# Kernel optimization log

Measured on AMD Instinct MI355X. Metric: run time of the kernel, lower is better.

## Reference

```python
import jax, jax.numpy as jnp
import numpy as np

D_IN = 128
D_HID = 256


def _mlp(x, W1, b1, W2, b2):
    # two-layer MLP with ReLU (dropout is identity at eval)
    h = jax.nn.relu(x @ W1 + b1)
    return jax.nn.relu(h @ W2 + b2)


def setup_inputs() -> dict:
    key = jax.random.key(0)
    kA, kB, k1, k2, k3, k4 = jax.random.split(key, 6)
    A = jax.random.normal(kA, (4, 4096, D_IN), dtype=jnp.float32)
    B = jax.random.normal(kB, (4, 4096, D_IN), dtype=jnp.float32)
    s1 = 1.0 / np.sqrt(D_IN)
    s2 = 1.0 / np.sqrt(D_HID)
    W1 = jax.random.uniform(k1, (D_IN, D_HID), jnp.float32, -s1, s1)
    b1 = jax.random.uniform(k2, (D_HID,), jnp.float32, -s1, s1)
    W2 = jax.random.uniform(k3, (D_HID, D_HID), jnp.float32, -s2, s2)
    b2 = jax.random.uniform(k4, (D_HID,), jnp.float32, -s2, s2)
    return {"A": A, "B": B, "W1": W1, "b1": b1, "W2": W2, "b2": b2}


def reference(A, B, W1, b1, W2, b2):
    f_A = _mlp(A, W1, b1, W2, b2)  # [b, m, h]
    f_B = _mlp(B, W1, b1, W2, b2)  # [b, n, h]
    e = jnp.einsum('bmh,bnh->bmn', f_A, f_B)  # unscaled scores
    beta = jnp.einsum('bmn,bnd->bmd', jax.nn.softmax(e, axis=-1), B)
    alpha = jnp.einsum('bmn,bmd->bnd', jax.nn.softmax(e, axis=-2), A)
    return (beta, alpha)
```

## Files before the change

### kernel.cpp

```cpp
#include <hip/hip_runtime.h>

typedef __attribute__((ext_vector_type(8))) short bf16x8;
typedef __attribute__((ext_vector_type(4))) float f32x4;
typedef __attribute__((ext_vector_type(16))) float f32x16;

__device__ __forceinline__ ushort f2bf(float x) {
  union { float f; unsigned u; } c; c.f = x;
  unsigned u = c.u;
  u += 0x7fffu + ((u >> 16) & 1u);
  return (ushort)(u >> 16);
}

__device__ __forceinline__ unsigned cvt_pk_bf16(float lo, float hi) {
  unsigned r;
  asm("v_cvt_pk_bf16_f32 %0, %1, %2" : "=v"(r) : "v"(lo), "v"(hi));
  return r;
}

__device__ __forceinline__ void gl_lds16(const void* g, void* s) {
  __builtin_amdgcn_global_load_lds(
      (const __attribute__((address_space(1))) unsigned*)g,
      (__attribute__((address_space(3))) unsigned*)s, 16, 0, 0);
}

__global__ __launch_bounds__(256) void prep_w(
    const float* __restrict__ W1, const float* __restrict__ W2,
    ushort* __restrict__ Wt1, ushort* __restrict__ Wt2)
{
  int idx = blockIdx.x * 256 + threadIdx.x;
  if (idx < 32768) {
    int k = idx >> 8, n = idx & 255;
    Wt1[n * 128 + k] = f2bf(W1[idx]);
  }
  {
    int k = idx >> 8, n = idx & 255;
    Wt2[n * 256 + k] = f2bf(W2[idx]);
  }
}

__global__ __launch_bounds__(256) void fused_mlp(
    const float* __restrict__ A, const float* __restrict__ Bm,
    const ushort* __restrict__ Wt1, const float* __restrict__ b1,
    const ushort* __restrict__ Wt2, const float* __restrict__ b2,
    ushort* __restrict__ fA, ushort* __restrict__ fB,
    ushort* __restrict__ At, ushort* __restrict__ Bt)
{
  const float* X = blockIdx.y ? Bm : A;
  ushort* outF = blockIdx.y ? fB : fA;
  ushort* outT = blockIdx.y ? Bt : At;

  __shared__ ushort Xl[64][136];
  __shared__ ushort Hl[64][264];

  int tid = threadIdx.x;
  int l = tid & 63, w = tid >> 6;
  int rowbase = blockIdx.x * 64 + w * 16;

  bf16x8 xf[4];
  {
    int r = rowbase + (l & 15);
    int koff = (l >> 4) * 8;
    const float* Xp = X + (size_t)r * 128 + koff;
#pragma unroll
    for (int kc = 0; kc < 4; ++kc) {
      float4 a = *(const float4*)(Xp + kc * 32);
      float4 c = *(const float4*)(Xp + kc * 32 + 4);
      bf16x8 v;
      v[0] = (short)f2bf(a.x); v[1] = (short)f2bf(a.y);
      v[2] = (short)f2bf(a.z); v[3] = (short)f2bf(a.w);
      v[4] = (short)f2bf(c.x); v[5] = (short)f2bf(c.y);
      v[6] = (short)f2bf(c.z); v[7] = (short)f2bf(c.w);
      xf[kc] = v;
      *(bf16x8*)&Xl[w * 16 + (l & 15)][koff + kc * 32] = v;
    }
  }

  f32x4 acc1[16];
#pragma unroll
  for (int i = 0; i < 16; ++i) acc1[i] = (f32x4){0.f, 0.f, 0.f, 0.f};
#pragma unroll
  for (int kc = 0; kc < 4; ++kc) {
#pragma unroll
    for (int nf = 0; nf < 16; ++nf) {
      bf16x8 bfv = *(const bf16x8*)&Wt1[(size_t)(nf * 16 + (l & 15)) * 128 + kc * 32 + (l >> 4) * 8];
      acc1[nf] = __builtin_amdgcn_mfma_f32_16x16x32_bf16(xf[kc], bfv, acc1[nf], 0, 0, 0);
    }
  }
  __syncthreads();

  {
    int b = (blockIdx.x * 64) >> 12;
    int m0 = (blockIdx.x * 64) & 4095;
    int d = tid >> 1, mh = (tid & 1) * 32;
    ushort* op = outT + ((size_t)b * 128 + d) * 4096 + m0 + mh;
#pragma unroll
    for (int g = 0; g < 4; ++g) {
      bf16x8 v;
#pragma unroll
      for (int j = 0; j < 8; ++j) v[j] = (short)Xl[mh + g * 8 + j][d];
      *(bf16x8*)(op + g * 8) = v;
    }
  }

#pragma unroll
  for (int nf = 0; nf < 16; ++nf) {
    int col = nf * 16 + (l & 15);
    float bv = b1[col];
#pragma unroll
    for (int i = 0; i < 4; ++i) {
      float v = fmaxf(acc1[nf][i] + bv, 0.f);
      Hl[w * 16 + (l >> 4) * 4 + i][col] = f2bf(v);
    }
  }
  __syncthreads();

  bf16x8 hf[8];
  {
    int koff = (l >> 4) * 8;
#pragma unroll
    for (int kc = 0; kc < 8; ++kc)
      hf[kc] = *(const bf16x8*)&Hl[w * 16 + (l & 15)][koff + kc * 32];
  }
  f32x4 acc2[16];
#pragma unroll
  for (int i = 0; i < 16; ++i) acc2[i] = (f32x4){0.f, 0.f, 0.f, 0.f};
#pragma unroll
  for (int kc = 0; kc < 8; ++kc) {
#pragma unroll
    for (int nf = 0; nf < 16; ++nf) {
      bf16x8 bfv = *(const bf16x8*)&Wt2[(size_t)(nf * 16 + (l & 15)) * 256 + kc * 32 + (l >> 4) * 8];
      acc2[nf] = __builtin_amdgcn_mfma_f32_16x16x32_bf16(hf[kc], bfv, acc2[nf], 0, 0, 0);
    }
  }
#pragma unroll
  for (int nf = 0; nf < 16; ++nf) {
    int col = nf * 16 + (l & 15);
    float bv = b2[col];
#pragma unroll
    for (int i = 0; i < 4; ++i) {
      float v = fmaxf(acc2[nf][i] + bv, 0.f);
      outF[(size_t)(rowbase + (l >> 4) * 4 + i) * 256 + col] = f2bf(v);
    }
  }
}

__global__ __launch_bounds__(256, 2) void flash2(
    const ushort* __restrict__ fA, const ushort* __restrict__ fB,
    const ushort* __restrict__ At, const ushort* __restrict__ Bt,
    float* __restrict__ out)
{
  int bp = blockIdx.x;
  int pass = bp >> 2, b = bp & 3;
  int qbase = blockIdx.y * 64;
  const ushort* fQ = pass ? fB : fA;
  const ushort* fK = pass ? fA : fB;
  const ushort* Vg = pass ? At : Bt;
  float* O = out + (size_t)pass * (4u * 4096 * 128) + (size_t)b * 4096 * 128;

  __shared__ ushort Kl[2][64 * 256];

  int tid = threadIdx.x;
  int l = tid & 63, w = tid >> 6;
  int l31 = l & 31, g5 = l >> 5;
  int qw = w & 1, kw = w >> 1;

  const size_t fkbase = (size_t)b * 4096 * 256;
  const size_t vgbase = (size_t)b * 128 * 4096;

  auto stage_k = [&](int t_, int buf_) {
    const ushort* kp = fK + fkbase + (size_t)t_ * 16384;
    ushort* lb = &Kl[buf_][0] + w * 4096;
#pragma unroll
    for (int s = 0; s < 8; ++s) {
      int row = w * 16 + s * 2 + g5;
      int gs = l31 ^ (row & 7);
      gl_lds16(kp + (size_t)row * 256 + gs * 8, lb + s * 512);
    }
  };

  bf16x8 q[16];
  {
    const ushort* qp = fQ + fkbase + (size_t)(qbase + qw * 32 + l31) * 256 + g5 * 8;
#pragma unroll
    for (int kc = 0; kc < 16; ++kc) q[kc] = *(const bf16x8*)(qp + kc * 16);
  }

  f32x16 acc_o0 = {}, acc_o1 = {}, acc_o2 = {}, acc_o3 = {};
  float m_run = -INFINITY, l_run = 0.f;

  stage_k(0, 0);

  for (int t = 0; t < 64; ++t) {
    int cur = t & 1;
    __syncthreads();
    if (t < 63) stage_k(t + 1, cur ^ 1);

    bf16x8 vv[2][4];
#pragma unroll
    for (int dblk = 0; dblk < 4; ++dblk) {
      const ushort* vp = Vg + vgbase + (size_t)(dblk * 32 + l31) * 4096
                         + t * 64 + kw * 32 + g5 * 8;
#pragma unroll
      for (int kblk = 0; kblk < 2; ++kblk)
        vv[kblk][dblk] = *(const bf16x8*)(vp + kblk * 16);
    }

    const ushort* kbuf = &Kl[cur][0];
    int krow = kw * 32 + l31;
    int sx = l31 & 7;
    f32x16 s0 = {}, s1 = {};
#pragma unroll
    for (int kc = 0; kc < 8; ++kc) {
      bf16x8 a0 = *(const bf16x8*)&kbuf[krow * 256 + (((4 * kc + g5) ^ sx) * 8)];
      bf16x8 a1 = *(const bf16x8*)&kbuf[krow * 256 + (((4 * kc + 2 + g5) ^ sx) * 8)];
      s0 = __builtin_amdgcn_mfma_f32_32x32x16_bf16(a0, q[2 * kc],     s0, 0, 0, 0);
      s1 = __builtin_amdgcn_mfma_f32_32x32x16_bf16(a1, q[2 * kc + 1], s1, 0, 0, 0);
    }

    float sv[16];
#pragma unroll
    for (int r = 0; r < 16; ++r) sv[r] = s0[r] + s1[r];

    float pmax = sv[0];
#pragma unroll
    for (int r = 1; r < 16; ++r) pmax = fmaxf(pmax, sv[r]);
    pmax = fmaxf(pmax, __shfl_xor(pmax, 32));

    if (!__all(pmax <= m_run + 8.f)) {
      float mnew = fmaxf(m_run, pmax);
      float sc = __expf(m_run - mnew);
      l_run *= sc;
#pragma unroll
      for (int r = 0; r < 16; ++r) {
        float scr = __shfl(sc, (r & 3) + 8 * (r >> 2) + 4 * g5);
        acc_o0[r] *= scr; acc_o1[r] *= scr; acc_o2[r] *= scr; acc_o3[r] *= scr;
      }
      m_run = mnew;
    }

    float p[16], psum = 0.f;
#pragma unroll
    for (int r = 0; r < 16; ++r) {
      p[r] = __expf(sv[r] - m_run);
      psum += p[r];
    }
    l_run += psum + __shfl_xor(psum, 32);

    unsigned pk[4][2];
#pragma unroll
    for (int r2 = 0; r2 < 4; ++r2) {
      pk[r2][0] = cvt_pk_bf16(p[4 * r2 + 0], p[4 * r2 + 1]);
      pk[r2][1] = cvt_pk_bf16(p[4 * r2 + 2], p[4 * r2 + 3]);
    }

#pragma unroll
    for (int kblk = 0; kblk < 2; ++kblk) {
      int r2a = 2 * kblk, r2b = r2a + 1;
      unsigned la0 = pk[r2a][0], la1 = pk[r2a][1];
      unsigned lb0 = pk[r2b][0], lb1 = pk[r2b][1];
      unsigned s0w = g5 ? la0 : lb0, s1w = g5 ? la1 : lb1;
      unsigned rc0 = (unsigned)__shfl_xor((int)s0w, 32);
      unsigned rc1 = (unsigned)__shfl_xor((int)s1w, 32);
      union { unsigned u[4]; bf16x8 v; } pf;
      pf.u[0] = g5 ? rc0 : la0;  pf.u[1] = g5 ? rc1 : la1;
      pf.u[2] = g5 ? lb0 : rc0;  pf.u[3] = g5 ? lb1 : rc1;
      acc_o0 = __builtin_amdgcn_mfma_f32_32x32x16_bf16(pf.v, vv[kblk][0], acc_o0, 0, 0, 0);
      acc_o1 = __builtin_amdgcn_mfma_f32_32x32x16_bf16(pf.v, vv[kblk][1], acc_o1, 0, 0, 0);
      acc_o2 = __builtin_amdgcn_mfma_f32_32x32x16_bf16(pf.v, vv[kblk][2], acc_o2, 0, 0, 0);
      acc_o3 = __builtin_amdgcn_mfma_f32_32x32x16_bf16(pf.v, vv[kblk][3], acc_o3, 0, 0, 0);
    }
  }

  __syncthreads();
  float* shm = (float*)&Kl[0][0];
  shm[w * 128 + l] = m_run;
  shm[w * 128 + 64 + l] = l_run;
  {
    float* sa = shm + 512 + w * 2048;
    const f32x16& send0 = kw ? acc_o0 : acc_o2;
    const f32x16& send1 = kw ? acc_o1 : acc_o3;
#pragma unroll
    for (int r = 0; r < 16; ++r) {
      sa[r * 64 + l] = send0[r];
      sa[1024 + r * 64 + l] = send1[r];
    }
  }
  __syncthreads();
  {
    int pw = w ^ 2;
    float m1 = shm[pw * 128 + l];
    float l1 = shm[pw * 128 + 64 + l];
    float M = fmaxf(m_run, m1);
    float a0 = __expf(m_run - M), a1 = __expf(m1 - M);
    float inv = 1.f / (l_run * a0 + l1 * a1);
    const float* sp = shm + 512 + pw * 2048;
    const f32x16& keep0 = kw ? acc_o2 : acc_o0;
    const f32x16& keep1 = kw ? acc_o3 : acc_o1;
    int dbase = kw ? 64 : 0;
    int qr = qbase + qw * 32;
#pragma unroll
    for (int r = 0; r < 16; ++r) {
      int rowl = (r & 3) + 8 * (r >> 2) + 4 * g5;
      float invr = __shfl(inv, rowl);
      float a0r = __shfl(a0, rowl);
      float a1r = __shfl(a1, rowl);
      float* op = O + (size_t)(qr + rowl) * 128 + dbase + l31;
      op[0]  = (keep0[r] * a0r + sp[r * 64 + l] * a1r) * invr;
      op[32] = (keep1[r] * a0r + sp[1024 + r * 64 + l] * a1r) * invr;
    }
  }
}

extern "C" void kernel_launch(void* const* d_in, const int* in_sizes, int n_in,
                              void* d_out, int out_size, void* d_ws, size_t ws_size,
                              hipStream_t stream) {
  const float* A  = (const float*)d_in[0];
  const float* Bm = (const float*)d_in[1];
  const float* W1 = (const float*)d_in[2];
  const float* b1 = (const float*)d_in[3];
  const float* W2 = (const float*)d_in[4];
  const float* b2 = (const float*)d_in[5];
  float* out = (float*)d_out;

  ushort* ws = (ushort*)d_ws;
  ushort* fA  = ws;
  ushort* fB  = fA + 4194304;
  ushort* At  = fB + 4194304;
  ushort* Bt  = At + 2097152;
  ushort* Wt1 = Bt + 2097152;
  ushort* Wt2 = Wt1 + 32768;

  prep_w<<<256, 256, 0, stream>>>(W1, W2, Wt1, Wt2);
  fused_mlp<<<dim3(256, 2), 256, 0, stream>>>(A, Bm, Wt1, b1, Wt2, b2,
                                              fA, fB, At, Bt);
  flash2<<<dim3(8, 64), 256, 0, stream>>>(fA, fB, At, Bt, out);
}
```

Before: 233.3 us.

## Split flash attention over key chunks with fp16 partials and merge kernel

Replaces the single flash kernel with a split-K variant. Each block now has 512 threads, 128 query rows and one quarter of the keys. Each block writes normalized fp16 partial outputs plus per-row max and sum to workspace, and a separate merge kernel combines the four partials with log-sum-exp weights. The two passes run as separate launches that reuse the same partial buffers. The aim is more parallelism and fewer serial key iterations per block. The cost is extra global traffic, four launches instead of one, and fp16 rounding of the partial results.

```diff
diff --git a/kernel.cpp b/kernel.cpp
--- a/kernel.cpp
+++ b/kernel.cpp
@@ -144,45 +144,49 @@
   }
 }
 
-__global__ __launch_bounds__(256, 2) void flash2(
+__global__ __launch_bounds__(512, 4) void flashV(
     const ushort* __restrict__ fA, const ushort* __restrict__ fB,
     const ushort* __restrict__ At, const ushort* __restrict__ Bt,
-    float* __restrict__ out)
+    _Float16* __restrict__ Pf16, float* __restrict__ pML, int pass)
 {
-  int bp = blockIdx.x;
-  int pass = bp >> 2, b = bp & 3;
-  int qbase = blockIdx.y * 64;
+  int bx = blockIdx.x;
+  int b = bx >> 2, kc = bx & 3;
+  int qblk = blockIdx.y;
   const ushort* fQ = pass ? fB : fA;
   const ushort* fK = pass ? fA : fB;
   const ushort* Vg = pass ? At : Bt;
-  float* O = out + (size_t)pass * (4u * 4096 * 128) + (size_t)b * 4096 * 128;
-
-  __shared__ ushort Kl[2][64 * 256];
+  _Float16* P = Pf16 + (size_t)kc * 2097152 + (size_t)b * 524288;
+  float* pml = pML + ((size_t)kc * 4 + b) * 8192;
+
+  __shared__ ushort Kl[2][16384];
+  __shared__ float mlsh[1024];
 
   int tid = threadIdx.x;
   int l = tid & 63, w = tid >> 6;
   int l31 = l & 31, g5 = l >> 5;
-  int qw = w & 1, kw = w >> 1;
+  int qg = w >> 1, kw = w & 1;
 
   const size_t fkbase = (size_t)b * 4096 * 256;
   const size_t vgbase = (size_t)b * 128 * 4096;
+  const int key0 = kc * 1024;
 
   auto stage_k = [&](int t_, int buf_) {
-    const ushort* kp = fK + fkbase + (size_t)t_ * 16384;
-    ushort* lb = &Kl[buf_][0] + w * 4096;
-#pragma unroll
-    for (int s = 0; s < 8; ++s) {
-      int row = w * 16 + s * 2 + g5;
-      int gs = l31 ^ (row & 7);
+    const ushort* kp = fK + fkbase + (size_t)(key0 + t_ * 64) * 256;
+    ushort* lb = &Kl[buf_][0] + w * 2048;
+#pragma unroll
+    for (int s = 0; s < 4; ++s) {
+      int row = w * 8 + s * 2 + g5;
+      int gs = l31 ^ (row & 31);
       gl_lds16(kp + (size_t)row * 256 + gs * 8, lb + s * 512);
     }
   };
 
   bf16x8 q[16];
   {
-    const ushort* qp = fQ + fkbase + (size_t)(qbase + qw * 32 + l31) * 256 + g5 * 8;
-#pragma unroll
-    for (int kc = 0; kc < 16; ++kc) q[kc] = *(const bf16x8*)(qp + kc * 16);
+    const ushort* qp = fQ + fkbase
+        + (size_t)(qblk * 128 + qg * 32 + l31) * 256 + g5 * 8;
+#pragma unroll
+    for (int kq = 0; kq < 16; ++kq) q[kq] = *(const bf16x8*)(qp + kq * 16);
   }
 
   f32x16 acc_o0 = {}, acc_o1 = {}, acc_o2 = {}, acc_o3 = {};
@@ -190,31 +194,29 @@
 
   stage_k(0, 0);
 
-  for (int t = 0; t < 64; ++t) {
+  for (int t = 0; t < 16; ++t) {
     int cur = t & 1;
     __syncthreads();
-    if (t < 63) stage_k(t + 1, cur ^ 1);
+    if (t < 15) stage_k(t + 1, cur ^ 1);
 
     bf16x8 vv[2][4];
 #pragma unroll
     for (int dblk = 0; dblk < 4; ++dblk) {
       const ushort* vp = Vg + vgbase + (size_t)(dblk * 32 + l31) * 4096
-                         + t * 64 + kw * 32 + g5 * 8;
-#pragma unroll
-      for (int kblk = 0; kblk < 2; ++kblk)
-        vv[kblk][dblk] = *(const bf16x8*)(vp + kblk * 16);
+                         + key0 + t * 64 + kw * 32 + g5 * 8;
+      vv[0][dblk] = *(const bf16x8*)(vp);
+      vv[1][dblk] = *(const bf16x8*)(vp + 16);
     }
 
     const ushort* kbuf = &Kl[cur][0];
     int krow = kw * 32 + l31;
-    int sx = l31 & 7;
     f32x16 s0 = {}, s1 = {};
 #pragma unroll
-    for (int kc = 0; kc < 8; ++kc) {
-      bf16x8 a0 = *(const bf16x8*)&kbuf[krow * 256 + (((4 * kc + g5) ^ sx) * 8)];
-      bf16x8 a1 = *(const bf16x8*)&kbuf[krow * 256 + (((4 * kc + 2 + g5) ^ sx) * 8)];
-      s0 = __builtin_amdgcn_mfma_f32_32x32x16_bf16(a0, q[2 * kc],     s0, 0, 0, 0);
-      s1 = __builtin_amdgcn_mfma_f32_32x32x16_bf16(a1, q[2 * kc + 1], s1, 0, 0, 0);
+    for (int kq = 0; kq < 8; ++kq) {
+      bf16x8 a0 = *(const bf16x8*)&kbuf[krow * 256 + (((4 * kq + g5)     ^ l31) * 8)];
+      bf16x8 a1 = *(const bf16x8*)&kbuf[krow * 256 + (((4 * kq + 2 + g5) ^ l31) * 8)];
+      s0 = __builtin_amdgcn_mfma_f32_32x32x16_bf16(a0, q[2 * kq],     s0, 0, 0, 0);
+      s1 = __builtin_amdgcn_mfma_f32_32x32x16_bf16(a1, q[2 * kq + 1], s1, 0, 0, 0);
     }
 
     float sv[16];
@@ -272,11 +274,11 @@
   }
 
   __syncthreads();
-  float* shm = (float*)&Kl[0][0];
-  shm[w * 128 + l] = m_run;
-  shm[w * 128 + 64 + l] = l_run;
-  {
-    float* sa = shm + 512 + w * 2048;
+  mlsh[w * 128 + l] = m_run;
+  mlsh[w * 128 + 64 + l] = l_run;
+  float* accsh = (float*)&Kl[0][0];
+  {
+    float* sa = accsh + w * 2048;
     const f32x16& send0 = kw ? acc_o0 : acc_o2;
     const f32x16& send1 = kw ? acc_o1 : acc_o3;
 #pragma unroll
@@ -287,28 +289,65 @@
   }
   __syncthreads();
   {
-    int pw = w ^ 2;
-    float m1 = shm[pw * 128 + l];
-    float l1 = shm[pw * 128 + 64 + l];
+    int pw = w ^ 1;
+    float m1 = mlsh[pw * 128 + l];
+    float l1 = mlsh[pw * 128 + 64 + l];
     float M = fmaxf(m_run, m1);
     float a0 = __expf(m_run - M), a1 = __expf(m1 - M);
-    float inv = 1.f / (l_run * a0 + l1 * a1);
-    const float* sp = shm + 512 + pw * 2048;
+    float lsum = l_run * a0 + l1 * a1;
+    float inv = 1.f / lsum;
+    const float* sp = accsh + pw * 2048;
     const f32x16& keep0 = kw ? acc_o2 : acc_o0;
     const f32x16& keep1 = kw ? acc_o3 : acc_o1;
     int dbase = kw ? 64 : 0;
-    int qr = qbase + qw * 32;
+    int qr = qblk * 128 + qg * 32;
+    if (kw == 0 && g5 == 0) {
+      pml[qr + l31] = M;
+      pml[4096 + qr + l31] = lsum;
+    }
 #pragma unroll
     for (int r = 0; r < 16; ++r) {
       int rowl = (r & 3) + 8 * (r >> 2) + 4 * g5;
       float invr = __shfl(inv, rowl);
       float a0r = __shfl(a0, rowl);
       float a1r = __shfl(a1, rowl);
-      float* op = O + (size_t)(qr + rowl) * 128 + dbase + l31;
-      op[0]  = (keep0[r] * a0r + sp[r * 64 + l] * a1r) * invr;
-      op[32] = (keep1[r] * a0r + sp[1024 + r * 64 + l] * a1r) * invr;
-    }
-  }
+      _Float16* op = P + (size_t)(qr + rowl) * 128 + dbase + l31;
+      op[0]  = (_Float16)((keep0[r] * a0r + sp[r * 64 + l] * a1r) * invr);
+      op[32] = (_Float16)((keep1[r] * a0r + sp[1024 + r * 64 + l] * a1r) * invr);
+    }
+  }
+}
+
+__global__ __launch_bounds__(256) void kmerge4(
+    float* __restrict__ outp, const _Float16* __restrict__ Pf16,
+    const float* __restrict__ pML)
+{
+  size_t i = ((size_t)blockIdx.x * 256 + threadIdx.x) * 4;
+  int fr = (int)(i >> 7);
+  int b = fr >> 12, row = fr & 4095;
+
+  float m0 = pML[((size_t)0 * 4 + b) * 8192 + row];
+  float m1 = pML[((size_t)1 * 4 + b) * 8192 + row];
+  float m2 = pML[((size_t)2 * 4 + b) * 8192 + row];
+  float m3 = pML[((size_t)3 * 4 + b) * 8192 + row];
+  float M = fmaxf(fmaxf(m0, m1), fmaxf(m2, m3));
+  float w0 = __expf(m0 - M) * pML[((size_t)0 * 4 + b) * 8192 + 4096 + row];
+  float w1 = __expf(m1 - M) * pML[((size_t)1 * 4 + b) * 8192 + 4096 + row];
+  float w2 = __expf(m2 - M) * pML[((size_t)2 * 4 + b) * 8192 + 4096 + row];
+  float w3 = __expf(m3 - M) * pML[((size_t)3 * 4 + b) * 8192 + 4096 + row];
+  float inv = 1.f / (w0 + w1 + w2 + w3);
+
+  typedef __attribute__((ext_vector_type(4))) _Float16 f16x4;
+  f16x4 p0 = *(const f16x4*)(Pf16 + 0 * 2097152 + i);
+  f16x4 p1 = *(const f16x4*)(Pf16 + 1 * 2097152 + i);
+  f16x4 p2 = *(const f16x4*)(Pf16 + 2 * 2097152 + i);
+  f16x4 p3 = *(const f16x4*)(Pf16 + 3 * 2097152 + i);
+  f32x4 r;
+#pragma unroll
+  for (int j = 0; j < 4; ++j)
+    r[j] = (w0 * (float)p0[j] + w1 * (float)p1[j] +
+            w2 * (float)p2[j] + w3 * (float)p3[j]) * inv;
+  *(f32x4*)(outp + i) = r;
 }
 
 extern "C" void kernel_launch(void* const* d_in, const int* in_sizes, int n_in,
@@ -329,9 +368,14 @@
   ushort* Bt  = At + 2097152;
   ushort* Wt1 = Bt + 2097152;
   ushort* Wt2 = Wt1 + 32768;
+  _Float16* Pf16 = (_Float16*)(Wt2 + 65536);
+  float* pML = (float*)(Pf16 + 8388608);
 
   prep_w<<<256, 256, 0, stream>>>(W1, W2, Wt1, Wt2);
   fused_mlp<<<dim3(256, 2), 256, 0, stream>>>(A, Bm, Wt1, b1, Wt2, b2,
                                               fA, fB, At, Bt);
-  flash2<<<dim3(8, 64), 256, 0, stream>>>(fA, fB, At, Bt, out);
-}
+  flashV<<<dim3(16, 32), 512, 0, stream>>>(fA, fB, At, Bt, Pf16, pML, 0);
+  kmerge4<<<2048, 256, 0, stream>>>(out, Pf16, pML);
+  flashV<<<dim3(16, 32), 512, 0, stream>>>(fA, fB, At, Bt, Pf16, pML, 1);
+  kmerge4<<<2048, 256, 0, stream>>>(out + 2097152, Pf16, pML);
+}
```

Result: slower. 630.5 us (+170.3%).
